# Kernel optimization log

Measured on AMD Instinct MI355X. Metric: run time of the kernel, lower is better.

## Reference

```python
import jax, jax.numpy as jnp
import numpy as np

N_NODES = 50000
N_EDGES = 800000
F_IN = 128
HID = 128
N_CLASSES = 2
N_GRAPHS = 500
NEG_SLOPE = 0.2


def setup_inputs() -> dict:
    key = jax.random.key(0)
    ks = jax.random.split(key, 16)
    inp = {
        "x": jax.random.normal(ks[0], (N_NODES, F_IN), dtype=jnp.float32),
        "edge_index": jax.random.randint(ks[1], (2, N_EDGES), 0, N_NODES, dtype=jnp.int64),
        "batch": jnp.sort(jax.random.randint(ks[2], (N_NODES,), 0, N_GRAPHS, dtype=jnp.int64)),
    }
    dims = [(F_IN, HID), (HID, HID), (HID, HID)]
    for i, (din, dout) in enumerate(dims, start=1):
        s = 1.0 / np.sqrt(din)
        inp[f"W{i}"] = jax.random.uniform(ks[3 * i], (din, dout), minval=-s, maxval=s, dtype=jnp.float32)
        inp[f"a_src{i}"] = jax.random.uniform(ks[3 * i + 1], (dout,), minval=-s, maxval=s, dtype=jnp.float32)
        inp[f"a_dst{i}"] = jax.random.uniform(ks[3 * i + 2], (dout,), minval=-s, maxval=s, dtype=jnp.float32)
        inp[f"b{i}"] = jnp.zeros((dout,), dtype=jnp.float32)
    s = 1.0 / np.sqrt(HID)
    inp["W_lin"] = jax.random.uniform(ks[12], (HID, N_CLASSES), minval=-s, maxval=s, dtype=jnp.float32)
    inp["b_lin"] = jax.random.uniform(ks[13], (N_CLASSES,), minval=-s, maxval=s, dtype=jnp.float32)
    return inp


def gat_conv(x, src, dst, W, a_src, a_dst, b, n_nodes):
    # single-head PyG GATConv (heads=1, concat), self-loops already in src/dst
    h = x @ W                                   # [N, dout]
    alpha_src = h @ a_src                       # [N]
    alpha_dst = h @ a_dst                       # [N]
    e = jax.nn.leaky_relu(alpha_src[src] + alpha_dst[dst], NEG_SLOPE)  # [E]
    # segment softmax over edges grouped by destination node
    m = jax.ops.segment_max(e, dst, num_segments=n_nodes)
    ex = jnp.exp(e - m[dst])
    denom = jax.ops.segment_sum(ex, dst, num_segments=n_nodes)
    alpha = ex / denom[dst]                     # [E]
    out = jax.ops.segment_sum(h[src] * alpha[:, None], dst, num_segments=n_nodes)
    return out + b


def reference(x, edge_index, batch, W1, a_src1, a_dst1, b1, W2, a_src2, a_dst2, b2,
              W3, a_src3, a_dst3, b3, W_lin, b_lin):
    n = x.shape[0]
    loops = jnp.arange(n, dtype=edge_index.dtype)
    src = jnp.concatenate([edge_index[0], loops])
    dst = jnp.concatenate([edge_index[1], loops])

    h = jax.nn.relu(gat_conv(x, src, dst, W1, a_src1, a_dst1, b1, n))
    h = jax.nn.relu(gat_conv(h, src, dst, W2, a_src2, a_dst2, b2, n))
    h = gat_conv(h, src, dst, W3, a_src3, a_dst3, b3, n)

    # global mean pool over graphs
    sums = jax.ops.segment_sum(h, batch, num_segments=N_GRAPHS)       # [G, HID]
    counts = jax.ops.segment_sum(jnp.ones((n,), h.dtype), batch, num_segments=N_GRAPHS)
    pooled = sums / jnp.maximum(counts, 1.0)[:, None]
    # dropout is identity in eval mode
    return pooled @ W_lin + b_lin
```

## Files before the change

### kernel.cpp

```cpp
#include <hip/hip_runtime.h>
#include <math.h>

#define N_NODES  50000
#define N_EDGES  800000
#define FDIM     128
#define N_GRAPHS 500
#define NEG_SLOPE 0.2f
#define EN_TOTAL (N_EDGES + N_NODES)
#define SCAN_NB ((N_NODES + 255) / 256)
#define GEMM_TILES (N_NODES / 16)
#define WT_COLS 144

typedef short bf16x8 __attribute__((ext_vector_type(8)));
typedef float f32x4 __attribute__((ext_vector_type(4)));

static __device__ __forceinline__ float lrelu(float x) {
    return x >= 0.f ? x : NEG_SLOPE * x;
}
static __device__ __forceinline__ unsigned short f2bf(float v) {
    unsigned int u = __float_as_uint(v);
    u += 0x7fffu + ((u >> 16) & 1u);
    return (unsigned short)(u >> 16);
}
static __device__ __forceinline__ float bf2f(unsigned short s) {
    return __uint_as_float(((unsigned int)s) << 16);
}

__global__ __launch_bounds__(256) void prep_planes(
    const float* __restrict__ X, unsigned short* __restrict__ hi,
    unsigned short* __restrict__ lo)
{
    const int total = N_NODES * FDIM / 4;
    for (int i = blockIdx.x * 256 + threadIdx.x; i < total; i += gridDim.x * 256) {
        const float4 v = ((const float4*)X)[i];
        ushort4 h4, l4;
        h4.x = f2bf(v.x); l4.x = f2bf(v.x - bf2f(h4.x));
        h4.y = f2bf(v.y); l4.y = f2bf(v.y - bf2f(h4.y));
        h4.z = f2bf(v.z); l4.z = f2bf(v.z - bf2f(h4.z));
        h4.w = f2bf(v.w); l4.w = f2bf(v.w - bf2f(h4.w));
        ((ushort4*)hi)[i] = h4;
        ((ushort4*)lo)[i] = l4;
    }
}

__global__ __launch_bounds__(256) void prep_wt(
    const float* __restrict__ W0, const float* __restrict__ W1,
    const float* __restrict__ W2,
    const float* __restrict__ as0, const float* __restrict__ as1,
    const float* __restrict__ as2,
    const float* __restrict__ ad0, const float* __restrict__ ad1,
    const float* __restrict__ ad2,
    unsigned short* __restrict__ WT)
{
    const int l = blockIdx.x;
    const float* W  = (l == 0) ? W0  : (l == 1) ? W1  : W2;
    const float* As = (l == 0) ? as0 : (l == 1) ? as1 : as2;
    const float* Ad = (l == 0) ? ad0 : (l == 1) ? ad1 : ad2;
    unsigned short* hi = WT + (size_t)l * 2 * WT_COLS * FDIM;
    unsigned short* lo = hi + WT_COLS * FDIM;
    const int tid = threadIdx.x;

    __shared__ float wa[256];
    {
        const int k = tid & 127;
        const float* av = (tid < 128) ? As : Ad;
        float s = 0.f;
        for (int c = 0; c < 128; ++c) s += W[k * FDIM + c] * av[c];
        wa[tid] = s;
    }
    __syncthreads();

    for (int i = tid; i < FDIM * FDIM; i += 256) {
        const int k = i >> 7, c = i & 127;
        const float v = W[i];
        const unsigned short h = f2bf(v);
        hi[c * FDIM + k] = h;
        lo[c * FDIM + k] = f2bf(v - bf2f(h));
    }
    for (int k = tid; k < FDIM; k += 256) {
        const float vs = wa[k], vd = wa[128 + k];
        const unsigned short hs = f2bf(vs), hd = f2bf(vd);
        hi[128 * FDIM + k] = hs; lo[128 * FDIM + k] = f2bf(vs - bf2f(hs));
        hi[129 * FDIM + k] = hd; lo[129 * FDIM + k] = f2bf(vd - bf2f(hd));
    }
    for (int i = tid; i < 14 * FDIM; i += 256) {
        hi[130 * FDIM + i] = 0;
        lo[130 * FDIM + i] = 0;
    }
}

__global__ __launch_bounds__(256) void gemm_mfma4(
    const unsigned short* __restrict__ Ahi, const unsigned short* __restrict__ Alo,
    const unsigned short* __restrict__ WThi, const unsigned short* __restrict__ WTlo,
    unsigned short* __restrict__ Hb, float* __restrict__ asrcN, float* __restrict__ adstN)
{
    const int tid = threadIdx.x, wv = tid >> 6, lane = tid & 63;
    const int r16 = lane & 15, g = lane >> 4;
    const int t0 = wv * 2;

    bf16x8 bh[2][4], bl[2][4];
    #pragma unroll
    for (int tt = 0; tt < 2; ++tt) {
        const int c = (t0 + tt) * 16 + r16;
        #pragma unroll
        for (int cc = 0; cc < 4; ++cc) {
            bh[tt][cc] = *(const bf16x8*)(WThi + c * FDIM + cc * 32 + 8 * g);
            bl[tt][cc] = *(const bf16x8*)(WTlo + c * FDIM + cc * 32 + 8 * g);
        }
    }
    const unsigned short* WThiE = WThi + (128 + r16) * FDIM + 8 * g;
    const unsigned short* WTloE = WTlo + (128 + r16) * FDIM + 8 * g;

    int rot = 0;
    for (int tile = blockIdx.x; tile < GEMM_TILES; tile += gridDim.x, ++rot) {
        const int m0 = tile * 16;
        const size_t ra = (size_t)(m0 + r16) * FDIM;

        bf16x8 ah[4], al[4];
        #pragma unroll
        for (int cc = 0; cc < 4; ++cc) {
            ah[cc] = *(const bf16x8*)(Ahi + ra + cc * 32 + 8 * g);
            al[cc] = *(const bf16x8*)(Alo + ra + cc * 32 + 8 * g);
        }

        f32x4 acc0 = {0.f, 0.f, 0.f, 0.f}, acc1 = {0.f, 0.f, 0.f, 0.f};
        #pragma unroll
        for (int cc = 0; cc < 4; ++cc) {
            acc0 = __builtin_amdgcn_mfma_f32_16x16x32_bf16(ah[cc], bh[0][cc], acc0, 0, 0, 0);
            acc1 = __builtin_amdgcn_mfma_f32_16x16x32_bf16(ah[cc], bh[1][cc], acc1, 0, 0, 0);
            acc0 = __builtin_amdgcn_mfma_f32_16x16x32_bf16(al[cc], bh[0][cc], acc0, 0, 0, 0);
            acc1 = __builtin_amdgcn_mfma_f32_16x16x32_bf16(al[cc], bh[1][cc], acc1, 0, 0, 0);
            acc0 = __builtin_amdgcn_mfma_f32_16x16x32_bf16(ah[cc], bl[0][cc], acc0, 0, 0, 0);
            acc1 = __builtin_amdgcn_mfma_f32_16x16x32_bf16(ah[cc], bl[1][cc], acc1, 0, 0, 0);
        }

        const int rowb = m0 + 4 * g;
        #pragma unroll
        for (int r = 0; r < 4; ++r) {
            Hb[(size_t)(rowb + r) * FDIM + (t0 + 0) * 16 + r16] = f2bf(acc0[r]);
            Hb[(size_t)(rowb + r) * FDIM + (t0 + 1) * 16 + r16] = f2bf(acc1[r]);
        }

        if (wv == ((tile + rot) & 3)) {
            f32x4 acce = {0.f, 0.f, 0.f, 0.f};
            #pragma unroll
            for (int cc = 0; cc < 4; ++cc) {
                const bf16x8 bhe = *(const bf16x8*)(WThiE + cc * 32);
                const bf16x8 ble = *(const bf16x8*)(WTloE + cc * 32);
                acce = __builtin_amdgcn_mfma_f32_16x16x32_bf16(ah[cc], bhe, acce, 0, 0, 0);
                acce = __builtin_amdgcn_mfma_f32_16x16x32_bf16(al[cc], bhe, acce, 0, 0, 0);
                acce = __builtin_amdgcn_mfma_f32_16x16x32_bf16(ah[cc], ble, acce, 0, 0, 0);
            }
            if (r16 == 0) {
                #pragma unroll
                for (int r = 0; r < 4; ++r) asrcN[rowb + r] = acce[r];
            } else if (r16 == 1) {
                #pragma unroll
                for (int r = 0; r < 4; ++r) adstN[rowb + r] = acce[r];
            }
        }
    }
}

__global__ void count_edges(const int* __restrict__ ei, int* __restrict__ cnt) {
    int i = blockIdx.x * 256 + threadIdx.x;
    if (i < EN_TOTAL) {
        int d = (i < N_EDGES) ? ei[N_EDGES + i] : (i - N_EDGES);
        atomicAdd(&cnt[d], 1);
    }
}

__global__ __launch_bounds__(256) void scan_block(const int* __restrict__ cnt,
                                                  int* __restrict__ off,
                                                  int* __restrict__ blockSums) {
    __shared__ int s[256];
    const int i = blockIdx.x * 256 + threadIdx.x;
    s[threadIdx.x] = (i < N_NODES) ? cnt[i] : 0;
    __syncthreads();
    #pragma unroll
    for (int d = 1; d < 256; d <<= 1) {
        int t = (threadIdx.x >= d) ? s[threadIdx.x - d] : 0;
        __syncthreads();
        s[threadIdx.x] += t;
        __syncthreads();
    }
    if (i < N_NODES) off[i + 1] = s[threadIdx.x];
    if (threadIdx.x == 255) blockSums[blockIdx.x] = s[255];
}

__global__ __launch_bounds__(256) void scan_sums(int* __restrict__ blockSums) {
    __shared__ int s[256];
    s[threadIdx.x] = (threadIdx.x < SCAN_NB) ? blockSums[threadIdx.x] : 0;
    __syncthreads();
    #pragma unroll
    for (int d = 1; d < 256; d <<= 1) {
        int t = (threadIdx.x >= d) ? s[threadIdx.x - d] : 0;
        __syncthreads();
        s[threadIdx.x] += t;
        __syncthreads();
    }
    if (threadIdx.x < SCAN_NB)
        blockSums[threadIdx.x] = (threadIdx.x == 0) ? 0 : s[threadIdx.x - 1];
}

__global__ __launch_bounds__(256) void add_base(int* __restrict__ off,
                                                const int* __restrict__ blockSums) {
    const int i = blockIdx.x * 256 + threadIdx.x;
    if (i < N_NODES) off[i + 1] += blockSums[blockIdx.x];
    if (i == 0) off[0] = 0;
}

__global__ void scatter_edges(const int* __restrict__ ei, const int* __restrict__ off,
                              int* __restrict__ cur, int* __restrict__ srcs) {
    int i = blockIdx.x * 256 + threadIdx.x;
    if (i < EN_TOTAL) {
        int s, d;
        if (i < N_EDGES) { s = ei[i]; d = ei[N_EDGES + i]; }
        else             { s = d = i - N_EDGES; }
        int p = off[d] + atomicAdd(&cur[d], 1);
        srcs[p] = s;
    }
}

__global__ __launch_bounds__(256) void gat_aggregate(
    const unsigned short* __restrict__ Hb, const int* __restrict__ off,
    const int* __restrict__ srcs,
    const float* __restrict__ asrcN, const float* __restrict__ adstN,
    const float* __restrict__ bias,
    unsigned short* __restrict__ PHI, unsigned short* __restrict__ PLO,
    float* __restrict__ OUTF, int mode)
{
    const int wave = threadIdx.x >> 6, lane = threadIdx.x & 63;
    const int grp = lane >> 3, fl = lane & 7;

    for (int n = blockIdx.x * 4 + wave; n < N_NODES; n += gridDim.x * 4) {
        const int s0 = off[n], s1 = off[n + 1];
        const int deg = s1 - s0;
        const float ad = adstN[n];

        float e_reg = -1e30f;
        float m = -1e30f;
        for (int j = s0 + lane; j < s1; j += 64) {
            float e = lrelu(asrcN[srcs[j]] + ad);
            if (j - s0 < 64) e_reg = e;
            m = fmaxf(m, e);
        }
        #pragma unroll
        for (int o = 32; o; o >>= 1) m = fmaxf(m, __shfl_xor(m, o));

        float4 a0 = {0,0,0,0}, a1 = {0,0,0,0}, a2 = {0,0,0,0}, a3 = {0,0,0,0};
        float dn = 0.f;
        const unsigned short* Hf = Hb + (size_t)fl * 16;
        for (int j = s0 + grp; j < s1; j += 8) {
            const int s = srcs[j];
            const float ex = (deg <= 64)
                ? __expf(__shfl(e_reg, j - s0) - m)
                : __expf(lrelu(asrcN[s] + ad) - m);
            dn += ex;
            const uint4* hp = (const uint4*)(Hf + (size_t)s * FDIM);
            const uint4 u0 = hp[0], u1 = hp[1];
            a0.x += ex * __uint_as_float(u0.x << 16);
            a0.y += ex * __uint_as_float(u0.x & 0xffff0000u);
            a0.z += ex * __uint_as_float(u0.y << 16);
            a0.w += ex * __uint_as_float(u0.y & 0xffff0000u);
            a1.x += ex * __uint_as_float(u0.z << 16);
            a1.y += ex * __uint_as_float(u0.z & 0xffff0000u);
            a1.z += ex * __uint_as_float(u0.w << 16);
            a1.w += ex * __uint_as_float(u0.w & 0xffff0000u);
            a2.x += ex * __uint_as_float(u1.x << 16);
            a2.y += ex * __uint_as_float(u1.x & 0xffff0000u);
            a2.z += ex * __uint_as_float(u1.y << 16);
            a2.w += ex * __uint_as_float(u1.y & 0xffff0000u);
            a3.x += ex * __uint_as_float(u1.z << 16);
            a3.y += ex * __uint_as_float(u1.z & 0xffff0000u);
            a3.z += ex * __uint_as_float(u1.w << 16);
            a3.w += ex * __uint_as_float(u1.w & 0xffff0000u);
        }

        #pragma unroll
        for (int o = 8; o <= 32; o <<= 1) {
            dn  += __shfl_xor(dn, o);
            a0.x += __shfl_xor(a0.x, o); a0.y += __shfl_xor(a0.y, o);
            a0.z += __shfl_xor(a0.z, o); a0.w += __shfl_xor(a0.w, o);
            a1.x += __shfl_xor(a1.x, o); a1.y += __shfl_xor(a1.y, o);
            a1.z += __shfl_xor(a1.z, o); a1.w += __shfl_xor(a1.w, o);
            a2.x += __shfl_xor(a2.x, o); a2.y += __shfl_xor(a2.y, o);
            a2.z += __shfl_xor(a2.z, o); a2.w += __shfl_xor(a2.w, o);
            a3.x += __shfl_xor(a3.x, o); a3.y += __shfl_xor(a3.y, o);
            a3.z += __shfl_xor(a3.z, o); a3.w += __shfl_xor(a3.w, o);
        }

        if (grp == 0) {
            const float rd = 1.f / dn;
            const float4* bp = (const float4*)(bias + fl * 16);
            float4 ov[4] = {a0, a1, a2, a3};
            #pragma unroll
            for (int q = 0; q < 4; ++q) {
                const float4 b4 = bp[q];
                float4 o4;
                o4.x = ov[q].x * rd + b4.x; o4.y = ov[q].y * rd + b4.y;
                o4.z = ov[q].z * rd + b4.z; o4.w = ov[q].w * rd + b4.w;
                if (mode == 0) {
                    o4.x = fmaxf(o4.x, 0.f); o4.y = fmaxf(o4.y, 0.f);
                    o4.z = fmaxf(o4.z, 0.f); o4.w = fmaxf(o4.w, 0.f);
                    ushort4 h4, l4;
                    h4.x = f2bf(o4.x); l4.x = f2bf(o4.x - bf2f(h4.x));
                    h4.y = f2bf(o4.y); l4.y = f2bf(o4.y - bf2f(h4.y));
                    h4.z = f2bf(o4.z); l4.z = f2bf(o4.z - bf2f(h4.z));
                    h4.w = f2bf(o4.w); l4.w = f2bf(o4.w - bf2f(h4.w));
                    const size_t base = (size_t)n * FDIM + fl * 16 + q * 4;
                    *(ushort4*)(PHI + base) = h4;
                    *(ushort4*)(PLO + base) = l4;
                } else {
                    *(float4*)(OUTF + (size_t)n * FDIM + fl * 16 + q * 4) = o4;
                }
            }
        }
    }
}

__global__ __launch_bounds__(256) void pool_linear2(
    const float* __restrict__ H, const int* __restrict__ batch,
    const float* __restrict__ Wlin, const float* __restrict__ blin,
    float* __restrict__ out)
{
    const int g = blockIdx.x, tid = threadIdx.x;
    const int rl = tid >> 5, fq = tid & 31;

    int a = 0, b = N_NODES;
    while (a < b) { int mid = (a + b) >> 1; if (batch[mid] < g) a = mid + 1; else b = mid; }
    const int lo = a;
    b = N_NODES;
    while (a < b) { int mid = (a + b) >> 1; if (batch[mid] <= g) a = mid + 1; else b = mid; }
    const int hi = a;

    float4 acc = {0.f, 0.f, 0.f, 0.f};
    for (int n = lo + rl; n < hi; n += 8) {
        const float4 v = *(const float4*)(H + (size_t)n * FDIM + fq * 4);
        acc.x += v.x; acc.y += v.y; acc.z += v.z; acc.w += v.w;
    }
    __shared__ float4 s[8][32];
    s[rl][fq] = acc;
    __syncthreads();

    if (tid < 32) {
        float4 t = s[0][fq];
        #pragma unroll
        for (int r = 1; r < 8; ++r) {
            const float4 v = s[r][fq];
            t.x += v.x; t.y += v.y; t.z += v.z; t.w += v.w;
        }
        const float inv = 1.f / fmaxf((float)(hi - lo), 1.f);
        t.x *= inv; t.y *= inv; t.z *= inv; t.w *= inv;
        float d0 = t.x * Wlin[(fq * 4 + 0) * 2 + 0] + t.y * Wlin[(fq * 4 + 1) * 2 + 0]
                 + t.z * Wlin[(fq * 4 + 2) * 2 + 0] + t.w * Wlin[(fq * 4 + 3) * 2 + 0];
        float d1 = t.x * Wlin[(fq * 4 + 0) * 2 + 1] + t.y * Wlin[(fq * 4 + 1) * 2 + 1]
                 + t.z * Wlin[(fq * 4 + 2) * 2 + 1] + t.w * Wlin[(fq * 4 + 3) * 2 + 1];
        #pragma unroll
        for (int o = 1; o <= 16; o <<= 1) {
            d0 += __shfl_xor(d0, o);
            d1 += __shfl_xor(d1, o);
        }
        if (fq == 0) {
            out[g * 2 + 0] = d0 + blin[0];
            out[g * 2 + 1] = d1 + blin[1];
        }
    }
}

extern "C" void kernel_launch(void* const* d_in, const int* in_sizes, int n_in,
                              void* d_out, int out_size, void* d_ws, size_t ws_size,
                              hipStream_t stream)
{
    const float* x     = (const float*)d_in[0];
    const int*   ei    = (const int*)d_in[1];
    const int*   batch = (const int*)d_in[2];
    const float* W[3]    = {(const float*)d_in[3],  (const float*)d_in[7],  (const float*)d_in[11]};
    const float* avs[3]  = {(const float*)d_in[4],  (const float*)d_in[8],  (const float*)d_in[12]};
    const float* avd[3]  = {(const float*)d_in[5],  (const float*)d_in[9],  (const float*)d_in[13]};
    const float* bias[3] = {(const float*)d_in[6],  (const float*)d_in[10], (const float*)d_in[14]};
    const float* Wlin = (const float*)d_in[15];
    const float* blin = (const float*)d_in[16];
    float* out = (float*)d_out;

    char* w = (char*)d_ws;
    unsigned short* Ahi = (unsigned short*)w; w += (size_t)N_NODES * FDIM * 2;
    unsigned short* Alo = (unsigned short*)w; w += (size_t)N_NODES * FDIM * 2;
    float* hOf = (float*)Ahi;
    unsigned short* Hb = (unsigned short*)w; w += (size_t)N_NODES * FDIM * 2;
    float* attn  = (float*)w; w += 2 * 200192;
    int*   off   = (int*)w;   w += 200192;
    int*   cnt   = (int*)w;   w += 200192;
    int*   bsum  = (int*)w;   w += 4096;
    int*   srcs  = (int*)w;   w += (size_t)EN_TOTAL * 4;
    unsigned short* WT = (unsigned short*)w; w += (size_t)3 * 2 * WT_COLS * FDIM * 2;
    float* asrcN = attn;
    float* adstN = attn + N_NODES;

    prep_planes<<<1024, 256, 0, stream>>>(x, Ahi, Alo);
    prep_wt<<<3, 256, 0, stream>>>(W[0], W[1], W[2],
                                   avs[0], avs[1], avs[2],
                                   avd[0], avd[1], avd[2], WT);

    hipMemsetAsync(cnt, 0, N_NODES * sizeof(int), stream);
    count_edges<<<(EN_TOTAL + 255) / 256, 256, 0, stream>>>(ei, cnt);
    scan_block<<<SCAN_NB, 256, 0, stream>>>(cnt, off, bsum);
    scan_sums<<<1, 256, 0, stream>>>(bsum);
    add_base<<<SCAN_NB, 256, 0, stream>>>(off, bsum);
    hipMemsetAsync(cnt, 0, N_NODES * sizeof(int), stream);
    scatter_edges<<<(EN_TOTAL + 255) / 256, 256, 0, stream>>>(ei, off, cnt, srcs);

    for (int l = 0; l < 3; ++l) {
        const unsigned short* WThi = WT + (size_t)l * 2 * WT_COLS * FDIM;
        const unsigned short* WTlo = WThi + WT_COLS * FDIM;
        gemm_mfma4<<<1024, 256, 0, stream>>>(Ahi, Alo, WThi, WTlo, Hb, asrcN, adstN);
        gat_aggregate<<<2048, 256, 0, stream>>>(Hb, off, srcs, asrcN, adstN, bias[l],
                                                Ahi, Alo, hOf, (l < 2) ? 0 : 1);
    }

    pool_linear2<<<N_GRAPHS, 256, 0, stream>>>(hOf, batch, Wlin, blin, out);
}
```

Before: 355.9 us.

## Store GEMM A operand hi/lo planes in MFMA fragment-ordered interleaved layout

Replaces the two row-major bf16 hi/lo planes with one buffer laid out in the per-lane MFMA fragment order, with hi and lo chunks interleaved per tile. The GEMM loads each fragment as a contiguous 16-byte-per-lane stream instead of strided row reads. The prep kernel and the aggregate epilogue are rewritten to write this layout. The intent is fully coalesced A loads in the GEMM, at the cost of more scattered 16-byte writes in the aggregate epilogue and a more complex index mapping.

```diff
diff --git a/kernel.cpp b/kernel.cpp
--- a/kernel.cpp
+++ b/kernel.cpp
@@ -14,6 +14,7 @@
 typedef short bf16x8 __attribute__((ext_vector_type(8)));
 typedef float f32x4 __attribute__((ext_vector_type(4)));
 
+
 static __device__ __forceinline__ float lrelu(float x) {
     return x >= 0.f ? x : NEG_SLOPE * x;
 }
@@ -27,20 +28,28 @@
 }
 
 __global__ __launch_bounds__(256) void prep_planes(
-    const float* __restrict__ X, unsigned short* __restrict__ hi,
-    unsigned short* __restrict__ lo)
-{
-    const int total = N_NODES * FDIM / 4;
-    for (int i = blockIdx.x * 256 + threadIdx.x; i < total; i += gridDim.x * 256) {
-        const float4 v = ((const float4*)X)[i];
-        ushort4 h4, l4;
-        h4.x = f2bf(v.x); l4.x = f2bf(v.x - bf2f(h4.x));
-        h4.y = f2bf(v.y); l4.y = f2bf(v.y - bf2f(h4.y));
-        h4.z = f2bf(v.z); l4.z = f2bf(v.z - bf2f(h4.z));
-        h4.w = f2bf(v.w); l4.w = f2bf(v.w - bf2f(h4.w));
-        ((ushort4*)hi)[i] = h4;
-        ((ushort4*)lo)[i] = l4;
-    }
+    const float* __restrict__ X, unsigned short* __restrict__ Abuf)
+{
+    const int i = blockIdx.x * 256 + threadIdx.x;
+    if (i >= GEMM_TILES * 4 * 64) return;
+    const int tile = i >> 8, rem = i & 255;
+    const int cc = rem >> 6, lane = rem & 63;
+    const int r16 = lane & 15, g = lane >> 4;
+    const int row = tile * 16 + r16;
+    const int k0 = cc * 32 + g * 8;
+
+    const float4 v0 = *(const float4*)(X + (size_t)row * FDIM + k0);
+    const float4 v1 = *(const float4*)(X + (size_t)row * FDIM + k0 + 4);
+    const float vv[8] = {v0.x, v0.y, v0.z, v0.w, v1.x, v1.y, v1.z, v1.w};
+    unsigned short h8[8], l8[8];
+    #pragma unroll
+    for (int e = 0; e < 8; ++e) {
+        h8[e] = f2bf(vv[e]);
+        l8[e] = f2bf(vv[e] - bf2f(h8[e]));
+    }
+    const size_t base = ((size_t)(tile * 8 + cc * 2) * 64 + lane) * 8;
+    *(uint4*)(Abuf + base)            = *(const uint4*)h8;
+    *(uint4*)(Abuf + base + 64 * 8)   = *(const uint4*)l8;
 }
 
 __global__ __launch_bounds__(256) void prep_wt(
@@ -89,8 +98,8 @@
     }
 }
 
-__global__ __launch_bounds__(256) void gemm_mfma4(
-    const unsigned short* __restrict__ Ahi, const unsigned short* __restrict__ Alo,
+__global__ __launch_bounds__(256) void gemm_mfma5(
+    const unsigned short* __restrict__ Abuf,
     const unsigned short* __restrict__ WThi, const unsigned short* __restrict__ WTlo,
     unsigned short* __restrict__ Hb, float* __restrict__ asrcN, float* __restrict__ adstN)
 {
@@ -114,13 +123,13 @@
     int rot = 0;
     for (int tile = blockIdx.x; tile < GEMM_TILES; tile += gridDim.x, ++rot) {
         const int m0 = tile * 16;
-        const size_t ra = (size_t)(m0 + r16) * FDIM;
+        const bf16x8* At = (const bf16x8*)Abuf + (size_t)tile * 512 + lane;
 
         bf16x8 ah[4], al[4];
         #pragma unroll
         for (int cc = 0; cc < 4; ++cc) {
-            ah[cc] = *(const bf16x8*)(Ahi + ra + cc * 32 + 8 * g);
-            al[cc] = *(const bf16x8*)(Alo + ra + cc * 32 + 8 * g);
+            ah[cc] = At[cc * 128];
+            al[cc] = At[cc * 128 + 64];
         }
 
         f32x4 acc0 = {0.f, 0.f, 0.f, 0.f}, acc1 = {0.f, 0.f, 0.f, 0.f};
@@ -227,8 +236,7 @@
     const int* __restrict__ srcs,
     const float* __restrict__ asrcN, const float* __restrict__ adstN,
     const float* __restrict__ bias,
-    unsigned short* __restrict__ PHI, unsigned short* __restrict__ PLO,
-    float* __restrict__ OUTF, int mode)
+    unsigned short* __restrict__ Abuf, float* __restrict__ OUTF, int mode)
 {
     const int wave = threadIdx.x >> 6, lane = threadIdx.x & 63;
     const int grp = lane >> 3, fl = lane & 7;
@@ -294,6 +302,7 @@
             const float rd = 1.f / dn;
             const float4* bp = (const float4*)(bias + fl * 16);
             float4 ov[4] = {a0, a1, a2, a3};
+            float o16[16];
             #pragma unroll
             for (int q = 0; q < 4; ++q) {
                 const float4 b4 = bp[q];
@@ -303,16 +312,28 @@
                 if (mode == 0) {
                     o4.x = fmaxf(o4.x, 0.f); o4.y = fmaxf(o4.y, 0.f);
                     o4.z = fmaxf(o4.z, 0.f); o4.w = fmaxf(o4.w, 0.f);
-                    ushort4 h4, l4;
-                    h4.x = f2bf(o4.x); l4.x = f2bf(o4.x - bf2f(h4.x));
-                    h4.y = f2bf(o4.y); l4.y = f2bf(o4.y - bf2f(h4.y));
-                    h4.z = f2bf(o4.z); l4.z = f2bf(o4.z - bf2f(h4.z));
-                    h4.w = f2bf(o4.w); l4.w = f2bf(o4.w - bf2f(h4.w));
-                    const size_t base = (size_t)n * FDIM + fl * 16 + q * 4;
-                    *(ushort4*)(PHI + base) = h4;
-                    *(ushort4*)(PLO + base) = l4;
+                    o16[q * 4 + 0] = o4.x; o16[q * 4 + 1] = o4.y;
+                    o16[q * 4 + 2] = o4.z; o16[q * 4 + 3] = o4.w;
                 } else {
                     *(float4*)(OUTF + (size_t)n * FDIM + fl * 16 + q * 4) = o4;
+                }
+            }
+            if (mode == 0) {
+                const int tile = n >> 4, r16 = n & 15, cc = fl >> 1;
+                #pragma unroll
+                for (int jc = 0; jc < 2; ++jc) {
+                    unsigned short h8[8], l8[8];
+                    #pragma unroll
+                    for (int e = 0; e < 8; ++e) {
+                        const float v = o16[jc * 8 + e];
+                        h8[e] = f2bf(v);
+                        l8[e] = f2bf(v - bf2f(h8[e]));
+                    }
+                    const int gslot = (fl & 1) * 2 + jc;
+                    const size_t baseH = ((size_t)(tile * 8 + cc * 2 + 0) * 64 + gslot * 16 + r16) * 8;
+                    const size_t baseL = ((size_t)(tile * 8 + cc * 2 + 1) * 64 + gslot * 16 + r16) * 8;
+                    *(uint4*)(Abuf + baseH) = *(const uint4*)h8;
+                    *(uint4*)(Abuf + baseL) = *(const uint4*)l8;
                 }
             }
         }
@@ -384,9 +405,8 @@
     float* out = (float*)d_out;
 
     char* w = (char*)d_ws;
-    unsigned short* Ahi = (unsigned short*)w; w += (size_t)N_NODES * FDIM * 2;
-    unsigned short* Alo = (unsigned short*)w; w += (size_t)N_NODES * FDIM * 2;
-    float* hOf = (float*)Ahi;
+    unsigned short* Abuf = (unsigned short*)w; w += (size_t)N_NODES * FDIM * 4;
+    float* hOf = (float*)Abuf;
     unsigned short* Hb = (unsigned short*)w; w += (size_t)N_NODES * FDIM * 2;
     float* attn  = (float*)w; w += 2 * 200192;
     int*   off   = (int*)w;   w += 200192;
@@ -397,7 +417,7 @@
     float* asrcN = attn;
     float* adstN = attn + N_NODES;
 
-    prep_planes<<<1024, 256, 0, stream>>>(x, Ahi, Alo);
+    prep_planes<<<(GEMM_TILES * 4 * 64 + 255) / 256, 256, 0, stream>>>(x, Abuf);
     prep_wt<<<3, 256, 0, stream>>>(W[0], W[1], W[2],
                                    avs[0], avs[1], avs[2],
                                    avd[0], avd[1], avd[2], WT);
@@ -413,9 +433,9 @@
     for (int l = 0; l < 3; ++l) {
         const unsigned short* WThi = WT + (size_t)l * 2 * WT_COLS * FDIM;
         const unsigned short* WTlo = WThi + WT_COLS * FDIM;
-        gemm_mfma4<<<1024, 256, 0, stream>>>(Ahi, Alo, WThi, WTlo, Hb, asrcN, adstN);
+        gemm_mfma5<<<1024, 256, 0, stream>>>(Abuf, WThi, WTlo, Hb, asrcN, adstN);
         gat_aggregate<<<2048, 256, 0, stream>>>(Hb, off, srcs, asrcN, adstN, bias[l],
-                                                Ahi, Alo, hOf, (l < 2) ? 0 : 1);
+                                                Abuf, hOf, (l < 2) ? 0 : 1);
     }
 
     pool_linear2<<<N_GRAPHS, 256, 0, stream>>>(hOf, batch, Wlin, blin, out);
```

Measured after the change: 389.2 us. +9.4%, slower.

## Fuse prep kernels, double-buffer GEMM A tiles in LDS, simplify edge scatter

Applied to the files above, without the earlier changes.

Merges the weight-prep, plane-split and count-zeroing memset into one prep_all launch, which removes two launches and a memset. The GEMM now stages each 16-row A tile into swizzled double-buffered LDS with coalesced 16-byte loads, prefetching the next tile while the current one computes; this adds a block barrier per tile. The edge scatter uses a copy of the offsets as the atomic cursor, dropping the second memset and one extra load per edge.

```diff
diff --git a/kernel.cpp b/kernel.cpp
--- a/kernel.cpp
+++ b/kernel.cpp
@@ -10,6 +10,8 @@
 #define SCAN_NB ((N_NODES + 255) / 256)
 #define GEMM_TILES (N_NODES / 16)
 #define WT_COLS 144
+#define PREP_PLANE_BLOCKS 1024
+#define PREP_GRID (3 + PREP_PLANE_BLOCKS + SCAN_NB)
 
 typedef short bf16x8 __attribute__((ext_vector_type(8)));
 typedef float f32x4 __attribute__((ext_vector_type(4)));
@@ -26,74 +28,78 @@
     return __uint_as_float(((unsigned int)s) << 16);
 }
 
-__global__ __launch_bounds__(256) void prep_planes(
-    const float* __restrict__ X, unsigned short* __restrict__ hi,
-    unsigned short* __restrict__ lo)
-{
-    const int total = N_NODES * FDIM / 4;
-    for (int i = blockIdx.x * 256 + threadIdx.x; i < total; i += gridDim.x * 256) {
-        const float4 v = ((const float4*)X)[i];
-        ushort4 h4, l4;
-        h4.x = f2bf(v.x); l4.x = f2bf(v.x - bf2f(h4.x));
-        h4.y = f2bf(v.y); l4.y = f2bf(v.y - bf2f(h4.y));
-        h4.z = f2bf(v.z); l4.z = f2bf(v.z - bf2f(h4.z));
-        h4.w = f2bf(v.w); l4.w = f2bf(v.w - bf2f(h4.w));
-        ((ushort4*)hi)[i] = h4;
-        ((ushort4*)lo)[i] = l4;
-    }
-}
-
-__global__ __launch_bounds__(256) void prep_wt(
+__global__ __launch_bounds__(256) void prep_all(
+    const float* __restrict__ X,
     const float* __restrict__ W0, const float* __restrict__ W1,
     const float* __restrict__ W2,
     const float* __restrict__ as0, const float* __restrict__ as1,
     const float* __restrict__ as2,
     const float* __restrict__ ad0, const float* __restrict__ ad1,
     const float* __restrict__ ad2,
-    unsigned short* __restrict__ WT)
+    unsigned short* __restrict__ WT,
+    unsigned short* __restrict__ PHI, unsigned short* __restrict__ PLO,
+    int* __restrict__ cnt)
 {
-    const int l = blockIdx.x;
-    const float* W  = (l == 0) ? W0  : (l == 1) ? W1  : W2;
-    const float* As = (l == 0) ? as0 : (l == 1) ? as1 : as2;
-    const float* Ad = (l == 0) ? ad0 : (l == 1) ? ad1 : ad2;
-    unsigned short* hi = WT + (size_t)l * 2 * WT_COLS * FDIM;
-    unsigned short* lo = hi + WT_COLS * FDIM;
-    const int tid = threadIdx.x;
-
     __shared__ float wa[256];
-    {
-        const int k = tid & 127;
-        const float* av = (tid < 128) ? As : Ad;
-        float s = 0.f;
-        for (int c = 0; c < 128; ++c) s += W[k * FDIM + c] * av[c];
-        wa[tid] = s;
-    }
-    __syncthreads();
-
-    for (int i = tid; i < FDIM * FDIM; i += 256) {
-        const int k = i >> 7, c = i & 127;
-        const float v = W[i];
-        const unsigned short h = f2bf(v);
-        hi[c * FDIM + k] = h;
-        lo[c * FDIM + k] = f2bf(v - bf2f(h));
-    }
-    for (int k = tid; k < FDIM; k += 256) {
-        const float vs = wa[k], vd = wa[128 + k];
-        const unsigned short hs = f2bf(vs), hd = f2bf(vd);
-        hi[128 * FDIM + k] = hs; lo[128 * FDIM + k] = f2bf(vs - bf2f(hs));
-        hi[129 * FDIM + k] = hd; lo[129 * FDIM + k] = f2bf(vd - bf2f(hd));
-    }
-    for (int i = tid; i < 14 * FDIM; i += 256) {
-        hi[130 * FDIM + i] = 0;
-        lo[130 * FDIM + i] = 0;
-    }
-}
-
-__global__ __launch_bounds__(256) void gemm_mfma4(
-    const unsigned short* __restrict__ Ahi, const unsigned short* __restrict__ Alo,
+    const int b = blockIdx.x, tid = threadIdx.x;
+
+    if (b < 3) {
+        const float* W  = (b == 0) ? W0  : (b == 1) ? W1  : W2;
+        const float* As = (b == 0) ? as0 : (b == 1) ? as1 : as2;
+        const float* Ad = (b == 0) ? ad0 : (b == 1) ? ad1 : ad2;
+        unsigned short* hi = WT + (size_t)b * 2 * WT_COLS * FDIM;
+        unsigned short* lo = hi + WT_COLS * FDIM;
+        {
+            const int k = tid & 127;
+            const float* av = (tid < 128) ? As : Ad;
+            float s = 0.f;
+            for (int c = 0; c < 128; ++c) s += W[k * FDIM + c] * av[c];
+            wa[tid] = s;
+        }
+        __syncthreads();
+        for (int i = tid; i < FDIM * FDIM; i += 256) {
+            const int k = i >> 7, c = i & 127;
+            const float v = W[i];
+            const unsigned short h = f2bf(v);
+            hi[c * FDIM + k] = h;
+            lo[c * FDIM + k] = f2bf(v - bf2f(h));
+        }
+        for (int k = tid; k < FDIM; k += 256) {
+            const float vs = wa[k], vd = wa[128 + k];
+            const unsigned short hs = f2bf(vs), hd = f2bf(vd);
+            hi[128 * FDIM + k] = hs; lo[128 * FDIM + k] = f2bf(vs - bf2f(hs));
+            hi[129 * FDIM + k] = hd; lo[129 * FDIM + k] = f2bf(vd - bf2f(hd));
+        }
+        for (int i = tid; i < 14 * FDIM; i += 256) {
+            hi[130 * FDIM + i] = 0;
+            lo[130 * FDIM + i] = 0;
+        }
+    } else if (b < 3 + PREP_PLANE_BLOCKS) {
+        const int total = N_NODES * FDIM / 4;
+        for (int i = (b - 3) * 256 + tid; i < total; i += PREP_PLANE_BLOCKS * 256) {
+            const float4 v = ((const float4*)X)[i];
+            ushort4 h4, l4;
+            h4.x = f2bf(v.x); l4.x = f2bf(v.x - bf2f(h4.x));
+            h4.y = f2bf(v.y); l4.y = f2bf(v.y - bf2f(h4.y));
+            h4.z = f2bf(v.z); l4.z = f2bf(v.z - bf2f(h4.z));
+            h4.w = f2bf(v.w); l4.w = f2bf(v.w - bf2f(h4.w));
+            ((ushort4*)PHI)[i] = h4;
+            ((ushort4*)PLO)[i] = l4;
+        }
+    } else {
+        const int i = (b - 3 - PREP_PLANE_BLOCKS) * 256 + tid;
+        if (i < N_NODES) cnt[i] = 0;
+    }
+}
+
+__global__ __launch_bounds__(256) void gemm_mfma6(
+    const unsigned short* __restrict__ PHI, const unsigned short* __restrict__ PLO,
     const unsigned short* __restrict__ WThi, const unsigned short* __restrict__ WTlo,
     unsigned short* __restrict__ Hb, float* __restrict__ asrcN, float* __restrict__ adstN)
 {
+    __shared__ unsigned short sH[2][16 * 128];
+    __shared__ unsigned short sL[2][16 * 128];
+
     const int tid = threadIdx.x, wv = tid >> 6, lane = tid & 63;
     const int r16 = lane & 15, g = lane >> 4;
     const int t0 = wv * 2;
@@ -111,16 +117,35 @@
     const unsigned short* WThiE = WThi + (128 + r16) * FDIM + 8 * g;
     const unsigned short* WTloE = WTlo + (128 + r16) * FDIM + 8 * g;
 
-    int rot = 0;
-    for (int tile = blockIdx.x; tile < GEMM_TILES; tile += gridDim.x, ++rot) {
-        const int m0 = tile * 16;
-        const size_t ra = (size_t)(m0 + r16) * FDIM;
+    const int srow = wv * 4 + (lane >> 4);
+    const int sslot = lane & 15;
+    const int ldsOfs = srow * 128 + ((sslot ^ (srow & 7)) * 8);
+    const size_t gOfs0 = (size_t)srow * FDIM + sslot * 8;
+
+    int tile = blockIdx.x;
+    {
+        const size_t go = (size_t)tile * 16 * FDIM + gOfs0;
+        *(uint4*)(&sH[0][ldsOfs]) = *(const uint4*)(PHI + go);
+        *(uint4*)(&sL[0][ldsOfs]) = *(const uint4*)(PLO + go);
+    }
+    __syncthreads();
+
+    int cur = 0, rot = 0;
+    for (; tile < GEMM_TILES; tile += gridDim.x, ++rot) {
+        const int nxt = tile + (int)gridDim.x;
+        if (nxt < GEMM_TILES) {
+            const size_t go = (size_t)nxt * 16 * FDIM + gOfs0;
+            *(uint4*)(&sH[cur ^ 1][ldsOfs]) = *(const uint4*)(PHI + go);
+            *(uint4*)(&sL[cur ^ 1][ldsOfs]) = *(const uint4*)(PLO + go);
+        }
 
         bf16x8 ah[4], al[4];
         #pragma unroll
         for (int cc = 0; cc < 4; ++cc) {
-            ah[cc] = *(const bf16x8*)(Ahi + ra + cc * 32 + 8 * g);
-            al[cc] = *(const bf16x8*)(Alo + ra + cc * 32 + 8 * g);
+            const int p = (cc * 4 + g) ^ (r16 & 7);
+            const int ofs = r16 * 128 + p * 8;
+            ah[cc] = *(const bf16x8*)(&sH[cur][ofs]);
+            al[cc] = *(const bf16x8*)(&sL[cur][ofs]);
         }
 
         f32x4 acc0 = {0.f, 0.f, 0.f, 0.f}, acc1 = {0.f, 0.f, 0.f, 0.f};
@@ -134,6 +159,7 @@
             acc1 = __builtin_amdgcn_mfma_f32_16x16x32_bf16(ah[cc], bl[1][cc], acc1, 0, 0, 0);
         }
 
+        const int m0 = tile * 16;
         const int rowb = m0 + 4 * g;
         #pragma unroll
         for (int r = 0; r < 4; ++r) {
@@ -159,6 +185,9 @@
                 for (int r = 0; r < 4; ++r) adstN[rowb + r] = acce[r];
             }
         }
+
+        __syncthreads();
+        cur ^= 1;
     }
 }
 
@@ -204,20 +233,25 @@
 }
 
 __global__ __launch_bounds__(256) void add_base(int* __restrict__ off,
-                                                const int* __restrict__ blockSums) {
+                                                const int* __restrict__ blockSums,
+                                                int* __restrict__ offm) {
     const int i = blockIdx.x * 256 + threadIdx.x;
-    if (i < N_NODES) off[i + 1] += blockSums[blockIdx.x];
-    if (i == 0) off[0] = 0;
-}
-
-__global__ void scatter_edges(const int* __restrict__ ei, const int* __restrict__ off,
-                              int* __restrict__ cur, int* __restrict__ srcs) {
+    if (i < N_NODES) {
+        const int v = off[i + 1] + blockSums[blockIdx.x];
+        off[i + 1] = v;
+        offm[i + 1] = v;
+    }
+    if (i == 0) { off[0] = 0; offm[0] = 0; }
+}
+
+__global__ void scatter_edges(const int* __restrict__ ei, int* __restrict__ offm,
+                              int* __restrict__ srcs) {
     int i = blockIdx.x * 256 + threadIdx.x;
     if (i < EN_TOTAL) {
         int s, d;
         if (i < N_EDGES) { s = ei[i]; d = ei[N_EDGES + i]; }
         else             { s = d = i - N_EDGES; }
-        int p = off[d] + atomicAdd(&cur[d], 1);
+        int p = atomicAdd(&offm[d], 1);
         srcs[p] = s;
     }
 }
@@ -384,12 +418,13 @@
     float* out = (float*)d_out;
 
     char* w = (char*)d_ws;
-    unsigned short* Ahi = (unsigned short*)w; w += (size_t)N_NODES * FDIM * 2;
-    unsigned short* Alo = (unsigned short*)w; w += (size_t)N_NODES * FDIM * 2;
-    float* hOf = (float*)Ahi;
+    unsigned short* PHI = (unsigned short*)w; w += (size_t)N_NODES * FDIM * 2;
+    unsigned short* PLO = (unsigned short*)w; w += (size_t)N_NODES * FDIM * 2;
+    float* hOf = (float*)PHI;
     unsigned short* Hb = (unsigned short*)w; w += (size_t)N_NODES * FDIM * 2;
     float* attn  = (float*)w; w += 2 * 200192;
     int*   off   = (int*)w;   w += 200192;
+    int*   offm  = (int*)w;   w += 200192;
     int*   cnt   = (int*)w;   w += 200192;
     int*   bsum  = (int*)w;   w += 4096;
     int*   srcs  = (int*)w;   w += (size_t)EN_TOTAL * 4;
@@ -397,25 +432,23 @@
     float* asrcN = attn;
     float* adstN = attn + N_NODES;
 
-    prep_planes<<<1024, 256, 0, stream>>>(x, Ahi, Alo);
-    prep_wt<<<3, 256, 0, stream>>>(W[0], W[1], W[2],
-                                   avs[0], avs[1], avs[2],
-                                   avd[0], avd[1], avd[2], WT);
-
-    hipMemsetAsync(cnt, 0, N_NODES * sizeof(int), stream);
+    prep_all<<<PREP_GRID, 256, 0, stream>>>(x, W[0], W[1], W[2],
+                                            avs[0], avs[1], avs[2],
+                                            avd[0], avd[1], avd[2],
+                                            WT, PHI, PLO, cnt);
+
     count_edges<<<(EN_TOTAL + 255) / 256, 256, 0, stream>>>(ei, cnt);
     scan_block<<<SCAN_NB, 256, 0, stream>>>(cnt, off, bsum);
     scan_sums<<<1, 256, 0, stream>>>(bsum);
-    add_base<<<SCAN_NB, 256, 0, stream>>>(off, bsum);
-    hipMemsetAsync(cnt, 0, N_NODES * sizeof(int), stream);
-    scatter_edges<<<(EN_TOTAL + 255) / 256, 256, 0, stream>>>(ei, off, cnt, srcs);
+    add_base<<<SCAN_NB, 256, 0, stream>>>(off, bsum, offm);
+    scatter_edges<<<(EN_TOTAL + 255) / 256, 256, 0, stream>>>(ei, offm, srcs);
 
     for (int l = 0; l < 3; ++l) {
         const unsigned short* WThi = WT + (size_t)l * 2 * WT_COLS * FDIM;
         const unsigned short* WTlo = WThi + WT_COLS * FDIM;
-        gemm_mfma4<<<1024, 256, 0, stream>>>(Ahi, Alo, WThi, WTlo, Hb, asrcN, adstN);
+        gemm_mfma6<<<1024, 256, 0, stream>>>(PHI, PLO, WThi, WTlo, Hb, asrcN, adstN);
         gat_aggregate<<<2048, 256, 0, stream>>>(Hb, off, srcs, asrcN, adstN, bias[l],
-                                                Ahi, Alo, hOf, (l < 2) ? 0 : 1);
+                                                PHI, PLO, hOf, (l < 2) ? 0 : 1);
     }
 
     pool_linear2<<<N_GRAPHS, 256, 0, stream>>>(hOf, batch, Wlin, blin, out);
```

After: 350.3 us. No clear change (-1.6%).
